# Kernel tuning notes

Measured on AMD Instinct MI355X. Metric: run time of the kernel, lower is better.

Reference implementation:

```python
import jax, jax.numpy as jnp
import numpy as np

M, I, J = 524288, 16, 16


def setup_inputs() -> dict:
    key = jax.random.key(0)
    k1, k2, k3, k4 = jax.random.split(key, 4)
    h = jax.random.normal(k1, (2, 1, 1, I, J), dtype=jnp.float32)
    gi = jax.random.normal(k2, (2, M, 1, I), dtype=jnp.float32)
    gj = jax.random.normal(k3, (2, 1, M, J), dtype=jnp.float32)
    theta = jax.random.uniform(k4, (2, M), dtype=jnp.float32) * (2.0 * np.pi)
    return {"h": h, "gi": gi, "gj": gj, "theta": theta}


def reference(h, gi, gj, theta):
    # Theta = diag(cos(theta[0])) + 1j * diag(sin(theta[1])) -- diagonal, so the
    # per-(i,j) bilinear form gj_j @ Theta @ gi_i is an O(M) contraction.
    tre = jnp.cos(theta[0])  # [M]
    tim = jnp.sin(theta[1])  # [M]
    a, b = gj[0, 0], gj[1, 0]            # [M, J] real/imag of gj
    e, f = gi[0, :, 0, :], gi[1, :, 0, :]  # [M, I] real/imag of gi
    # u = Theta_diag * gj (complex elementwise along M)
    u_re = a * tre[:, None] - b * tim[:, None]  # [M, J]
    u_im = a * tim[:, None] + b * tre[:, None]  # [M, J]
    # out[i,j] = sum_m gi[m,i] * theta[m] * gj[m,j] (complex)
    out_re = jnp.einsum('mi,mj->ij', e, u_re) - jnp.einsum('mi,mj->ij', f, u_im)
    out_im = jnp.einsum('mi,mj->ij', e, u_im) + jnp.einsum('mi,mj->ij', f, u_re)
    # htilde = h + reflected path, then squeeze the singleton dims -> [2, I, J]
    return h[:, 0, 0] + jnp.stack([out_re, out_im], axis=0)
```

## Files before the change

kernel.cpp:

```cpp
#include <hip/hip_runtime.h>


constexpr int MDIM    = 524288;
constexpr int THREADS = 256;
constexpr int BLOCKS  = 1024;
constexpr int M_PER_B = MDIM / BLOCKS;
constexpr int M_PER_W = M_PER_B / 4;
constexpr int CHUNK   = 16;
constexpr int NCH     = M_PER_W / CHUNK;
constexpr int DEPTH   = 2;

constexpr int E_OFF = 0, F_OFF = 256, A_OFF = 512, B_OFF = 768;
constexpr int T0_OFF = 1024, T1_OFF = 1040;
constexpr int BUF_F  = 1056;
constexpr int WAVE_F = DEPTH * BUF_F;
constexpr int SMEM_F = 4 * WAVE_F;
static_assert(SMEM_F * sizeof(float) <= 40960, "need <= 40 KiB for 4 blocks/CU");
static_assert(NCH >= 3, "pipeline needs at least 3 chunks");

typedef float f32x2 __attribute__((ext_vector_type(2)));

#define AS1 __attribute__((address_space(1)))
#define AS3 __attribute__((address_space(3)))

__device__ __forceinline__ void cp16(const float* g, float* l) {
    __builtin_amdgcn_global_load_lds((const AS1 void*)g, (AS3 void*)l, 16, 0, 0);
}
__device__ __forceinline__ void cp4(const float* g, float* l) {
    __builtin_amdgcn_global_load_lds((const AS1 void*)g, (AS3 void*)l, 4, 0, 0);
}

__device__ __forceinline__ void stage(
    const float* e_g, const float* f_g, const float* a_g, const float* b_g,
    const float* t0_g, const float* t1_g, float* buf, int p, int lane)
{
    const size_t mo = (size_t)p * (CHUNK * 16);
    cp16(e_g + mo, buf + E_OFF);
    cp16(f_g + mo, buf + F_OFF);
    cp16(a_g + mo, buf + A_OFF);
    cp16(b_g + mo, buf + B_OFF);
    if (lane < 16) {
        cp4(t0_g + (size_t)p * CHUNK, buf + T0_OFF);
        cp4(t1_g + (size_t)p * CHUNK, buf + T1_OFF);
    }
}

__device__ __forceinline__ void compute_chunk(
    const float* buf, int slot, int i0, int j0,
    f32x2 (&are)[4][2], f32x2 (&aim)[4][2])
{
#pragma unroll
    for (int k = 0; k < 4; ++k) {
        const int ml = slot + 4 * k;
        const float4 e4 = *(const float4*)(buf + E_OFF + ml * 16 + i0);
        const float4 f4 = *(const float4*)(buf + F_OFF + ml * 16 + i0);
        const float4 a4 = *(const float4*)(buf + A_OFF + ml * 16 + j0);
        const float4 b4 = *(const float4*)(buf + B_OFF + ml * 16 + j0);
        const float c = __cosf(buf[T0_OFF + ml]);
        const float s = __sinf(buf[T1_OFF + ml]);
        const f32x2 cc = {c, c}, ss = {s, s};
        const f32x2 a01 = {a4.x, a4.y}, a23 = {a4.z, a4.w};
        const f32x2 b01 = {b4.x, b4.y}, b23 = {b4.z, b4.w};
        f32x2 ure[2], uim[2];
        ure[0] = __builtin_elementwise_fma(-b01, ss, a01 * cc);
        ure[1] = __builtin_elementwise_fma(-b23, ss, a23 * cc);
        uim[0] = __builtin_elementwise_fma( b01, cc, a01 * ss);
        uim[1] = __builtin_elementwise_fma( b23, cc, a23 * ss);
        const float ev[4] = {e4.x, e4.y, e4.z, e4.w};
        const float fv[4] = {f4.x, f4.y, f4.z, f4.w};
#pragma unroll
        for (int i = 0; i < 4; ++i) {
            const f32x2 ee = {ev[i], ev[i]};
            const f32x2 ff = {fv[i], fv[i]};
#pragma unroll
            for (int jp = 0; jp < 2; ++jp) {
                are[i][jp] = __builtin_elementwise_fma( ee, ure[jp], are[i][jp]);
                are[i][jp] = __builtin_elementwise_fma(-ff, uim[jp], are[i][jp]);
                aim[i][jp] = __builtin_elementwise_fma( ee, uim[jp], aim[i][jp]);
                aim[i][jp] = __builtin_elementwise_fma( ff, ure[jp], aim[i][jp]);
            }
        }
    }
}

template <bool USE_ATOMIC>
__device__ __forceinline__ void theta_body(
    const float* __restrict__ gi, const float* __restrict__ gj,
    const float* __restrict__ theta, float* __restrict__ dst)
{
    __shared__ float smem[SMEM_F];
    const int t    = threadIdx.x;
    const int wave = t >> 6;
    const int lane = t & 63;
    const int slot = (lane >> 4) & 3;
    const int tile = lane & 15;
    const int i0   = (tile >> 2) << 2;
    const int j0   = (tile & 3) << 2;
    const int m_w0 = blockIdx.x * M_PER_B + wave * M_PER_W;
    float* wbase   = smem + wave * WAVE_F;

    const float* e_g  = gi + (size_t)m_w0 * 16 + lane * 4;
    const float* f_g  = e_g + (size_t)MDIM * 16;
    const float* a_g  = gj + (size_t)m_w0 * 16 + lane * 4;
    const float* b_g  = a_g + (size_t)MDIM * 16;
    const float* t0_g = theta + m_w0 + lane;
    const float* t1_g = t0_g + MDIM;

    f32x2 are[4][2], aim[4][2];
#pragma unroll
    for (int i = 0; i < 4; ++i)
#pragma unroll
        for (int jp = 0; jp < 2; ++jp) { are[i][jp] = {0.f, 0.f}; aim[i][jp] = {0.f, 0.f}; }

    stage(e_g, f_g, a_g, b_g, t0_g, t1_g, wbase + 0 * BUF_F, 0, lane);
    stage(e_g, f_g, a_g, b_g, t0_g, t1_g, wbase + 1 * BUF_F, 1, lane);

    for (int c = 0; c < NCH - 2; ++c) {
        asm volatile("s_waitcnt vmcnt(6)" ::: "memory");
        compute_chunk(wbase + (c & 1) * BUF_F, slot, i0, j0, are, aim);
        asm volatile("s_waitcnt lgkmcnt(0)" ::: "memory");
        stage(e_g, f_g, a_g, b_g, t0_g, t1_g, wbase + (c & 1) * BUF_F, c + 2, lane);
    }
    asm volatile("s_waitcnt vmcnt(6)" ::: "memory");
    compute_chunk(wbase + ((NCH - 2) & 1) * BUF_F, slot, i0, j0, are, aim);
    asm volatile("s_waitcnt vmcnt(0)" ::: "memory");
    compute_chunk(wbase + ((NCH - 1) & 1) * BUF_F, slot, i0, j0, are, aim);

    float sre[4][4], sim[4][4];
#pragma unroll
    for (int i = 0; i < 4; ++i)
#pragma unroll
        for (int jp = 0; jp < 2; ++jp) {
            sre[i][jp * 2]     = are[i][jp].x;  sre[i][jp * 2 + 1] = are[i][jp].y;
            sim[i][jp * 2]     = aim[i][jp].x;  sim[i][jp * 2 + 1] = aim[i][jp].y;
        }

#pragma unroll
    for (int i = 0; i < 4; ++i)
#pragma unroll
        for (int j = 0; j < 4; ++j) {
            sre[i][j] += __shfl_xor(sre[i][j], 16);
            sre[i][j] += __shfl_xor(sre[i][j], 32);
            sim[i][j] += __shfl_xor(sim[i][j], 16);
            sim[i][j] += __shfl_xor(sim[i][j], 32);
        }

    __syncthreads();
    float (*red)[16][33] = (float (*)[16][33])smem;
    if (lane < 16) {
#pragma unroll
        for (int i = 0; i < 4; ++i)
#pragma unroll
            for (int j = 0; j < 4; ++j) {
                red[wave][lane][i * 4 + j]      = sre[i][j];
                red[wave][lane][16 + i * 4 + j] = sim[i][j];
            }
    }
    __syncthreads();

#pragma unroll
    for (int k = 0; k < 2; ++k) {
        const int idx = t * 2 + k;
        const int tl  = idx >> 5;
        const int v   = idx & 31;
        const float sum = red[0][tl][v] + red[1][tl][v] + red[2][tl][v] + red[3][tl][v];
        const int ii  = ((tl >> 2) << 2) + ((v & 15) >> 2);
        const int jj  = ((tl & 3) << 2) + (v & 3);
        const int off = ((v & 16) ? 256 : 0) + ii * 16 + jj;
        if (USE_ATOMIC) atomicAdd(dst + off, sum);
        else            dst[blockIdx.x * 512 + off] = sum;
    }
}

__global__ __launch_bounds__(THREADS) void theta_main_ws(
    const float* __restrict__ gi, const float* __restrict__ gj,
    const float* __restrict__ theta, float* __restrict__ partial)
{
    theta_body<false>(gi, gj, theta, partial);
}

__global__ __launch_bounds__(THREADS) void theta_main_atomic(
    const float* __restrict__ gi, const float* __restrict__ gj,
    const float* __restrict__ theta, float* __restrict__ out)
{
    theta_body<true>(gi, gj, theta, out);
}

__global__ __launch_bounds__(256) void theta_reduce(
    const float* __restrict__ h, const float* __restrict__ partial,
    float* __restrict__ out)
{
    const int w    = (blockIdx.x * 256 + threadIdx.x) >> 6;
    const int lane = threadIdx.x & 63;
    float s = 0.f;
#pragma unroll 4
    for (int j = 0; j < BLOCKS / 64; ++j)
        s += partial[(size_t)(j * 64 + lane) * 512 + w];
#pragma unroll
    for (int d = 1; d < 64; d <<= 1) s += __shfl_xor(s, d);
    if (lane == 0) out[w] = h[w] + s;
}

__global__ void theta_init(const float* __restrict__ h, float* __restrict__ out) {
    int k = blockIdx.x * blockDim.x + threadIdx.x;
    if (k < 512) out[k] = h[k];
}

extern "C" void kernel_launch(void* const* d_in, const int* in_sizes, int n_in,
                              void* d_out, int out_size, void* d_ws, size_t ws_size,
                              hipStream_t stream) {
    const float* h     = (const float*)d_in[0];
    const float* gi    = (const float*)d_in[1];
    const float* gj    = (const float*)d_in[2];
    const float* theta = (const float*)d_in[3];
    float* out = (float*)d_out;

    const size_t need = (size_t)BLOCKS * 512 * sizeof(float);
    if (ws_size >= need) {
        float* partial = (float*)d_ws;
        theta_main_ws<<<BLOCKS, THREADS, 0, stream>>>(gi, gj, theta, partial);
        theta_reduce<<<128, 256, 0, stream>>>(h, partial, out);
    } else {
        theta_init<<<2, 256, 0, stream>>>(h, out);
        theta_main_atomic<<<BLOCKS, THREADS, 0, stream>>>(gi, gj, theta, out);
    }
}
```

Baseline: 165.2 us.

## Replace LDS async staging pipeline with direct global-to-register chunk loads

Drops the double-buffered global_load_lds staging and its manual waitcnt pipeline. Each lane now loads its own float4 slices of gi, gj and theta straight into registers per chunk, and lanes in the same slot fetch the same rows with different column offsets, so the cache sees redundant requests. The per-slot row assignment changes from interleaved to contiguous, a separate small shared array is used for the final reduction, and launch bounds now request 4 blocks per CU. The aim is to cut LDS traffic and synchronisation overhead, at the cost of duplicated vector-memory requests and relying on the compiler and occupancy for latency hiding.

```diff
diff --git a/kernel.cpp b/kernel.cpp
--- a/kernel.cpp
+++ b/kernel.cpp
@@ -8,57 +8,46 @@
 constexpr int M_PER_W = M_PER_B / 4;
 constexpr int CHUNK   = 16;
 constexpr int NCH     = M_PER_W / CHUNK;
-constexpr int DEPTH   = 2;
-
-constexpr int E_OFF = 0, F_OFF = 256, A_OFF = 512, B_OFF = 768;
-constexpr int T0_OFF = 1024, T1_OFF = 1040;
-constexpr int BUF_F  = 1056;
-constexpr int WAVE_F = DEPTH * BUF_F;
-constexpr int SMEM_F = 4 * WAVE_F;
-static_assert(SMEM_F * sizeof(float) <= 40960, "need <= 40 KiB for 4 blocks/CU");
-static_assert(NCH >= 3, "pipeline needs at least 3 chunks");
+static_assert(NCH * BLOCKS * 4 * CHUNK == MDIM, "exact tiling");
 
 typedef float f32x2 __attribute__((ext_vector_type(2)));
 
-#define AS1 __attribute__((address_space(1)))
-#define AS3 __attribute__((address_space(3)))
-
-__device__ __forceinline__ void cp16(const float* g, float* l) {
-    __builtin_amdgcn_global_load_lds((const AS1 void*)g, (AS3 void*)l, 16, 0, 0);
-}
-__device__ __forceinline__ void cp4(const float* g, float* l) {
-    __builtin_amdgcn_global_load_lds((const AS1 void*)g, (AS3 void*)l, 4, 0, 0);
-}
-
-__device__ __forceinline__ void stage(
-    const float* e_g, const float* f_g, const float* a_g, const float* b_g,
-    const float* t0_g, const float* t1_g, float* buf, int p, int lane)
-{
-    const size_t mo = (size_t)p * (CHUNK * 16);
-    cp16(e_g + mo, buf + E_OFF);
-    cp16(f_g + mo, buf + F_OFF);
-    cp16(a_g + mo, buf + A_OFF);
-    cp16(b_g + mo, buf + B_OFF);
-    if (lane < 16) {
-        cp4(t0_g + (size_t)p * CHUNK, buf + T0_OFF);
-        cp4(t1_g + (size_t)p * CHUNK, buf + T1_OFF);
-    }
+struct Chunk {
+    float4 e[4], f[4], a[4], b[4];
+    float4 t0, t1;
+};
+
+__device__ __forceinline__ void load_chunk(
+    Chunk& ch,
+    const float* __restrict__ e_g, const float* __restrict__ f_g,
+    const float* __restrict__ a_g, const float* __restrict__ b_g,
+    const float* __restrict__ t0_g, const float* __restrict__ t1_g,
+    size_t mb, int slot, int i0, int j0)
+{
+    const size_t mrow = mb + (size_t)slot * 4;
+#pragma unroll
+    for (int k = 0; k < 4; ++k) {
+        ch.e[k] = *(const float4*)(e_g + (mrow + k) * 16 + i0);
+        ch.f[k] = *(const float4*)(f_g + (mrow + k) * 16 + i0);
+        ch.a[k] = *(const float4*)(a_g + (mrow + k) * 16 + j0);
+        ch.b[k] = *(const float4*)(b_g + (mrow + k) * 16 + j0);
+    }
+    ch.t0 = *(const float4*)(t0_g + mrow);
+    ch.t1 = *(const float4*)(t1_g + mrow);
 }
 
 __device__ __forceinline__ void compute_chunk(
-    const float* buf, int slot, int i0, int j0,
-    f32x2 (&are)[4][2], f32x2 (&aim)[4][2])
-{
+    const Chunk& ch, f32x2 (&are)[4][2], f32x2 (&aim)[4][2])
+{
+    const float tc[4] = {ch.t0.x, ch.t0.y, ch.t0.z, ch.t0.w};
+    const float ts[4] = {ch.t1.x, ch.t1.y, ch.t1.z, ch.t1.w};
 #pragma unroll
     for (int k = 0; k < 4; ++k) {
-        const int ml = slot + 4 * k;
-        const float4 e4 = *(const float4*)(buf + E_OFF + ml * 16 + i0);
-        const float4 f4 = *(const float4*)(buf + F_OFF + ml * 16 + i0);
-        const float4 a4 = *(const float4*)(buf + A_OFF + ml * 16 + j0);
-        const float4 b4 = *(const float4*)(buf + B_OFF + ml * 16 + j0);
-        const float c = __cosf(buf[T0_OFF + ml]);
-        const float s = __sinf(buf[T1_OFF + ml]);
+        const float c = __cosf(tc[k]);
+        const float s = __sinf(ts[k]);
         const f32x2 cc = {c, c}, ss = {s, s};
+        const float4 a4 = ch.a[k], b4 = ch.b[k];
+        const float4 e4 = ch.e[k], f4 = ch.f[k];
         const f32x2 a01 = {a4.x, a4.y}, a23 = {a4.z, a4.w};
         const f32x2 b01 = {b4.x, b4.y}, b23 = {b4.z, b4.w};
         f32x2 ure[2], uim[2];
@@ -88,7 +77,6 @@
     const float* __restrict__ gi, const float* __restrict__ gj,
     const float* __restrict__ theta, float* __restrict__ dst)
 {
-    __shared__ float smem[SMEM_F];
     const int t    = threadIdx.x;
     const int wave = t >> 6;
     const int lane = t & 63;
@@ -96,15 +84,14 @@
     const int tile = lane & 15;
     const int i0   = (tile >> 2) << 2;
     const int j0   = (tile & 3) << 2;
-    const int m_w0 = blockIdx.x * M_PER_B + wave * M_PER_W;
-    float* wbase   = smem + wave * WAVE_F;
-
-    const float* e_g  = gi + (size_t)m_w0 * 16 + lane * 4;
-    const float* f_g  = e_g + (size_t)MDIM * 16;
-    const float* a_g  = gj + (size_t)m_w0 * 16 + lane * 4;
-    const float* b_g  = a_g + (size_t)MDIM * 16;
-    const float* t0_g = theta + m_w0 + lane;
-    const float* t1_g = t0_g + MDIM;
+    const size_t m0 = (size_t)(blockIdx.x * 4 + wave) * M_PER_W;
+
+    const float* e_g  = gi;
+    const float* f_g  = gi + (size_t)MDIM * 16;
+    const float* a_g  = gj;
+    const float* b_g  = gj + (size_t)MDIM * 16;
+    const float* t0_g = theta;
+    const float* t1_g = theta + MDIM;
 
     f32x2 are[4][2], aim[4][2];
 #pragma unroll
@@ -112,19 +99,12 @@
 #pragma unroll
         for (int jp = 0; jp < 2; ++jp) { are[i][jp] = {0.f, 0.f}; aim[i][jp] = {0.f, 0.f}; }
 
-    stage(e_g, f_g, a_g, b_g, t0_g, t1_g, wbase + 0 * BUF_F, 0, lane);
-    stage(e_g, f_g, a_g, b_g, t0_g, t1_g, wbase + 1 * BUF_F, 1, lane);
-
-    for (int c = 0; c < NCH - 2; ++c) {
-        asm volatile("s_waitcnt vmcnt(6)" ::: "memory");
-        compute_chunk(wbase + (c & 1) * BUF_F, slot, i0, j0, are, aim);
-        asm volatile("s_waitcnt lgkmcnt(0)" ::: "memory");
-        stage(e_g, f_g, a_g, b_g, t0_g, t1_g, wbase + (c & 1) * BUF_F, c + 2, lane);
-    }
-    asm volatile("s_waitcnt vmcnt(6)" ::: "memory");
-    compute_chunk(wbase + ((NCH - 2) & 1) * BUF_F, slot, i0, j0, are, aim);
-    asm volatile("s_waitcnt vmcnt(0)" ::: "memory");
-    compute_chunk(wbase + ((NCH - 1) & 1) * BUF_F, slot, i0, j0, are, aim);
+    for (int c = 0; c < NCH; ++c) {
+        Chunk ch;
+        load_chunk(ch, e_g, f_g, a_g, b_g, t0_g, t1_g,
+                   m0 + (size_t)c * CHUNK, slot, i0, j0);
+        compute_chunk(ch, are, aim);
+    }
 
     float sre[4][4], sim[4][4];
 #pragma unroll
@@ -145,8 +125,7 @@
             sim[i][j] += __shfl_xor(sim[i][j], 32);
         }
 
-    __syncthreads();
-    float (*red)[16][33] = (float (*)[16][33])smem;
+    __shared__ float red[4][16][33];
     if (lane < 16) {
 #pragma unroll
         for (int i = 0; i < 4; ++i)
@@ -172,14 +151,14 @@
     }
 }
 
-__global__ __launch_bounds__(THREADS) void theta_main_ws(
+__global__ __launch_bounds__(THREADS, 4) void theta_main_ws(
     const float* __restrict__ gi, const float* __restrict__ gj,
     const float* __restrict__ theta, float* __restrict__ partial)
 {
     theta_body<false>(gi, gj, theta, partial);
 }
 
-__global__ __launch_bounds__(THREADS) void theta_main_atomic(
+__global__ __launch_bounds__(THREADS, 4) void theta_main_atomic(
     const float* __restrict__ gi, const float* __restrict__ gj,
     const float* __restrict__ theta, float* __restrict__ out)
 {
```

After: 288.4 us. 1.75x slower.
